# Performance work log

Measured on AMD Instinct MI355X. Metric: run time of the kernel, lower is better.

The kernel has to match this reference:

```python
import jax, jax.numpy as jnp
import numpy as np
import math

# ---------------- static setup: real Clebsch-Gordan coefficients up to L=4 ----------------
L_MAX = 4
DIM = (L_MAX + 1) ** 2  # 25 irrep components
NUM_RADIAL = 64
R_CUT = 5.0
_DEG_OF = np.repeat(np.arange(L_MAX + 1), 2 * np.arange(L_MAX + 1) + 1)  # degree of each lm slot


def _cg_complex(l1, m1, l2, m2, l3, m3):
    if m1 + m2 != m3 or l3 < abs(l1 - l2) or l3 > l1 + l2:
        return 0.0
    f = math.factorial
    pref = math.sqrt((2 * l3 + 1) * f(l1 + l2 - l3) * f(l1 - l2 + l3) * f(-l1 + l2 + l3) / f(l1 + l2 + l3 + 1))
    pref *= math.sqrt(f(l1 + m1) * f(l1 - m1) * f(l2 + m2) * f(l2 - m2) * f(l3 + m3) * f(l3 - m3))
    s = 0.0
    for k in range(l1 + l2 - l3 + 1):
        d = (k, l1 + l2 - l3 - k, l1 - m1 - k, l2 + m2 - k, l3 - l2 + m1 + k, l3 - l1 - m2 + k)
        if min(d) < 0:
            continue
        den = 1
        for x in d:
            den *= f(x)
        s += (-1.0) ** k / den
    return pref * s


def _u_mat(l):
    # complex -> real spherical harmonics change of basis
    U = np.zeros((2 * l + 1, 2 * l + 1), dtype=np.complex128)
    U[l, l] = 1.0
    rs2 = 1.0 / math.sqrt(2.0)
    for m in range(1, l + 1):
        U[l + m, l + m] = (-1.0) ** m * rs2
        U[l + m, l - m] = rs2
        U[l - m, l - m] = 1j * rs2
        U[l - m, l + m] = -1j * (-1.0) ** m * rs2
    return U


def _real_cg():
    C = np.zeros((DIM, DIM, DIM))
    U = [_u_mat(l) for l in range(L_MAX + 1)]
    for l1 in range(L_MAX + 1):
        for l2 in range(L_MAX + 1):
            for l3 in range(L_MAX + 1):
                cgc = np.zeros((2 * l1 + 1, 2 * l2 + 1, 2 * l3 + 1))
                for m1 in range(-l1, l1 + 1):
                    for m2 in range(-l2, l2 + 1):
                        m3 = m1 + m2
                        if abs(m3) <= l3:
                            cgc[l1 + m1, l2 + m2, l3 + m3] = _cg_complex(l1, m1, l2, m2, l3, m3)
                blk = np.einsum('am,bn,cp,mnp->abc', U[l1], U[l2], U[l3].conj(), cgc.astype(np.complex128))
                blk = blk.real if (l1 + l2 + l3) % 2 == 0 else blk.imag
                C[l1 * l1:l1 * l1 + 2 * l1 + 1, l2 * l2:l2 * l2 + 2 * l2 + 1, l3 * l3:l3 * l3 + 2 * l3 + 1] = blk
    return C

_CG = jnp.asarray(_real_cg(), dtype=jnp.float32)  # [25,25,25]


def real_sh(u):
    # u: [P,3] unit vectors -> [P,25] orthonormal real spherical harmonics, L<=4
    x, y, z = u[:, 0], u[:, 1], u[:, 2]
    x2, y2, z2 = x * x, y * y, z * z
    Y = [jnp.full_like(x, 0.28209479177387814),
         0.4886025119029199 * y, 0.4886025119029199 * z, 0.4886025119029199 * x,
         1.0925484305920792 * x * y, 1.0925484305920792 * y * z,
         0.31539156525252005 * (3.0 * z2 - 1.0),
         1.0925484305920792 * x * z, 0.5462742152960396 * (x2 - y2),
         0.5900435899266435 * y * (3.0 * x2 - y2), 2.890611442640554 * x * y * z,
         0.4570457994644658 * y * (5.0 * z2 - 1.0), 0.3731763325901154 * z * (5.0 * z2 - 3.0),
         0.4570457994644658 * x * (5.0 * z2 - 1.0), 1.445305721320277 * z * (x2 - y2),
         0.5900435899266435 * x * (x2 - 3.0 * y2),
         2.5033429417967046 * x * y * (x2 - y2), 1.7701307697799304 * y * z * (3.0 * x2 - y2),
         0.9461746957575601 * x * y * (7.0 * z2 - 1.0), 0.6690465435572892 * y * z * (7.0 * z2 - 3.0),
         0.10578554691520431 * (35.0 * z2 * z2 - 30.0 * z2 + 3.0),
         0.6690465435572892 * x * z * (7.0 * z2 - 3.0), 0.47308734787878004 * (x2 - y2) * (7.0 * z2 - 1.0),
         1.7701307697799304 * x * z * (x2 - 3.0 * y2),
         0.6258357354491761 * (x2 * x2 - 6.0 * x2 * y2 + y2 * y2)]
    return jnp.stack(Y, axis=-1)


def deg_dense(feat, W, b):
    Wlm = W[_DEG_OF]  # [25,Fin,Fout]
    out = jnp.einsum('plf,lfg->plg', feat, Wlm)
    return out.at[:, 0, :].add(b)


def tensor_product(a, b):
    # channelwise CG coupling: out[p,k,f] = sum_ij CG[i,j,k] a[p,i,f] b[p,j,f]
    out = jnp.zeros_like(a)
    for i in range(DIM):  # fixed structural loop over 25 lm slots, avoids [P,25,25,F] temp
        out = out + a[:, i, None, :] * jnp.einsum('jk,pjf->pkf', _CG[i], b)
    return out


def radial_basis(disp, s_j):
    # species-aware radial basis x spherical harmonics -> [P,25,F]
    r = jnp.sqrt(jnp.sum(disp * disp, axis=-1) + 1e-12)
    Y = real_sh(disp / r[:, None])
    centers = jnp.linspace(0.0, R_CUT, NUM_RADIAL, dtype=disp.dtype)
    delta = R_CUT / (NUM_RADIAL - 1)
    g = jnp.exp(-0.5 / (delta * delta) * (r[:, None] - centers) ** 2)
    env = 0.5 * (jnp.cos(jnp.pi * jnp.clip(r / R_CUT, 0.0, 1.0)) + 1.0)  # smooth cutoff
    radial = g * env[:, None] * s_j  # species-modulated radial channels [P,F]
    return Y[:, :, None] * radial[:, None, :]


def setup_inputs() -> dict:
    key = jax.random.key(0)
    ks = jax.random.split(key, 8)
    num_atoms, num_pairs, F = 2048, 32768, 64
    return {
        'atomic_numbers': jax.random.randint(ks[0], (num_atoms,), 0, 119),
        'neighbour_displacements': jax.random.normal(ks[1], (num_pairs, 3), dtype=jnp.float32),
        'neighbour_indices': jax.random.randint(ks[2], (2, num_pairs), 0, num_atoms),
        'species_embed': jax.random.normal(ks[3], (119, F), dtype=jnp.float32),
        'Wt': jax.random.normal(ks[4], (F, F), dtype=jnp.float32) / 8.0,
        'bt': jnp.zeros((F,), dtype=jnp.float32),
        'W1': jax.random.normal(ks[5], (5, F, F), dtype=jnp.float32) / 8.0,
        'b1': jnp.zeros((F,), dtype=jnp.float32),
        'W2': jax.random.normal(ks[6], (5, F, F), dtype=jnp.float32) / 8.0,
        'b2': jnp.zeros((F,), dtype=jnp.float32),
    }


def reference(atomic_numbers, neighbour_displacements, neighbour_indices, species_embed, Wt, bt, W1, b1, W2, b2):
    idx_i, idx_j = neighbour_indices[0], neighbour_indices[1]
    s_j = species_embed[atomic_numbers[idx_j]]                 # gather Z_j embedding
    y = radial_basis(neighbour_displacements, s_j)             # [P,25,F]
    # TensorDense, applied max_moment-1 = 1 time
    y = tensor_product(deg_dense(y, W1, b1), deg_dense(y, W2, b2))
    # 'emb x basis': l1=0 CG is the identity -> channelwise scaling by scalar embedding of Z_i
    emb_i = species_embed[atomic_numbers[idx_i]] @ Wt + bt
    y = y * emb_i[:, None, :]
    out = jax.ops.segment_sum(y, idx_i, num_segments=atomic_numbers.shape[0])  # scatter-sum to atoms
    # residual: scalar embedding added to the l=0 component
    emb = species_embed[atomic_numbers] @ Wt + bt
    return out.at[:, 0, :].add(emb)
```

## Files before the change

kernel.cpp:

```cpp
#include <hip/hip_runtime.h>

#define DEVINL __device__ __forceinline__

typedef __attribute__((ext_vector_type(8))) short bf16x8;
typedef __attribute__((ext_vector_type(4))) float f32x4;

constexpr int LMAX = 4;

struct Triples { int n; int l1[80], l2[80], l3[80]; };
constexpr Triples make_triples() {
  Triples T{}; T.n = 0;
  for (int a = 0; a <= LMAX; ++a)
    for (int b = 0; b <= LMAX; ++b)
      for (int c = 0; c <= LMAX; ++c) {
        int lo = a > b ? a - b : b - a;
        if (c < lo || c > a + b) continue;
        T.l1[T.n] = a; T.l2[T.n] = b; T.l3[T.n] = c; ++T.n;
      }
  return T;
}
constexpr Triples TRI = make_triples();
static_assert(TRI.n == 65, "triples");

struct ETriT { int n; signed char l1[48], l2[48], l3[48]; };
constexpr ETriT make_etri() {
  ETriT E{}; E.n = 0;
  for (int t = 0; t < TRI.n; ++t)
    if (((TRI.l1[t] + TRI.l2[t] + TRI.l3[t]) & 1) == 0) {
      E.l1[E.n] = (signed char)TRI.l1[t];
      E.l2[E.n] = (signed char)TRI.l2[t];
      E.l3[E.n] = (signed char)TRI.l3[t];
      ++E.n;
    }
  return E;
}
constexpr ETriT ETRI = make_etri();
static_assert(ETRI.n == 42, "even triples");

constexpr double FT[14] = {1., 1., 2., 6., 24., 120., 720., 5040., 40320.,
                           362880., 3628800., 39916800., 479001600., 6227020800.};

constexpr double csqrt(double x) {
  if (x <= 0.0) return 0.0;
  double y = 1.0;
  while (y * y < x) y *= 2.0;
  for (int i = 0; i < 30; ++i) y = 0.5 * (y + x / y);
  return y;
}

constexpr double cg_complex(int l1, int m1, int l2, int m2, int l3, int m3) {
  if (m1 + m2 != m3) return 0.0;
  double pref = csqrt((2.0 * l3 + 1.0) * FT[l1 + l2 - l3] * FT[l1 - l2 + l3] *
                      FT[-l1 + l2 + l3] / FT[l1 + l2 + l3 + 1]);
  pref *= csqrt(FT[l1 + m1] * FT[l1 - m1] * FT[l2 + m2] * FT[l2 - m2] *
                FT[l3 + m3] * FT[l3 - m3]);
  double s = 0.0;
  for (int k = 0; k <= l1 + l2 - l3; ++k) {
    int d3 = l1 - m1 - k, d4 = l2 + m2 - k, d5 = l3 - l2 + m1 + k, d6 = l3 - l1 - m2 + k;
    if (d3 < 0 || d4 < 0 || d5 < 0 || d6 < 0) continue;
    double den = FT[k] * FT[l1 + l2 - l3 - k] * FT[d3] * FT[d4] * FT[d5] * FT[d6];
    s += ((k & 1) ? -1.0 : 1.0) / den;
  }
  return pref * s;
}

struct CURow { int n; int m[2]; double re[2], im[2]; };
constexpr CURow cu_row(int l, int a) {
  CURow u{}; int ma = a - l;
  const double RS2 = 0.70710678118654752440;
  if (ma == 0) { u.n = 1; u.m[0] = 0; u.re[0] = 1.0; u.im[0] = 0.0; }
  else if (ma > 0) {
    u.n = 2;
    u.m[0] = ma;  u.re[0] = ((ma & 1) ? -RS2 : RS2); u.im[0] = 0.0;
    u.m[1] = -ma; u.re[1] = RS2;                     u.im[1] = 0.0;
  } else {
    int mm = -ma; u.n = 2;
    u.m[0] = -mm; u.re[0] = 0.0; u.im[0] = RS2;
    u.m[1] =  mm; u.re[1] = 0.0; u.im[1] = ((mm & 1) ? RS2 : -RS2);
  }
  return u;
}

constexpr double real_cg_entry(int l1, int a, int l2, int b, int l3, int c) {
  CURow u1 = cu_row(l1, a), u2 = cu_row(l2, b), u3 = cu_row(l3, c);
  double sre = 0.0, sim = 0.0;
  for (int x = 0; x < u1.n; ++x)
    for (int y = 0; y < u2.n; ++y)
      for (int z = 0; z < u3.n; ++z) {
        int m1 = u1.m[x], m2 = u2.m[y], m3 = u3.m[z];
        if (m1 + m2 != m3) continue;
        double cg = cg_complex(l1, m1, l2, m2, l3, m3);
        if (cg == 0.0) continue;
        double are = u1.re[x], aim = u1.im[x], bre = u2.re[y], bim = u2.im[y];
        double pre = are * bre - aim * bim, pim = are * bim + aim * bre;
        double cre = u3.re[z], cim = -u3.im[z];
        sre += (pre * cre - pim * cim) * cg;
        sim += (pre * cim + pim * cre) * cg;
      }
  return ((l1 + l2 + l3) & 1) ? sim : sre;
}

struct Y25D { double y[25]; };
constexpr Y25D csh25(double x, double y, double z) {
  Y25D Y{};
  double x2 = x * x, y2 = y * y, z2 = z * z;
  Y.y[0] = 0.28209479177387814;
  Y.y[1] = 0.4886025119029199 * y;
  Y.y[2] = 0.4886025119029199 * z;
  Y.y[3] = 0.4886025119029199 * x;
  Y.y[4] = 1.0925484305920792 * x * y;
  Y.y[5] = 1.0925484305920792 * y * z;
  Y.y[6] = 0.31539156525252005 * (3.0 * z2 - 1.0);
  Y.y[7] = 1.0925484305920792 * x * z;
  Y.y[8] = 0.5462742152960396 * (x2 - y2);
  Y.y[9] = 0.5900435899266435 * y * (3.0 * x2 - y2);
  Y.y[10] = 2.890611442640554 * x * y * z;
  Y.y[11] = 0.4570457994644658 * y * (5.0 * z2 - 1.0);
  Y.y[12] = 0.3731763325901154 * z * (5.0 * z2 - 3.0);
  Y.y[13] = 0.4570457994644658 * x * (5.0 * z2 - 1.0);
  Y.y[14] = 1.445305721320277 * z * (x2 - y2);
  Y.y[15] = 0.5900435899266435 * x * (x2 - 3.0 * y2);
  Y.y[16] = 2.5033429417967046 * x * y * (x2 - y2);
  Y.y[17] = 1.7701307697799304 * y * z * (3.0 * x2 - y2);
  Y.y[18] = 0.9461746957575601 * x * y * (7.0 * z2 - 1.0);
  Y.y[19] = 0.6690465435572892 * y * z * (7.0 * z2 - 3.0);
  Y.y[20] = 0.10578554691520431 * (35.0 * z2 * z2 - 30.0 * z2 + 3.0);
  Y.y[21] = 0.6690465435572892 * x * z * (7.0 * z2 - 3.0);
  Y.y[22] = 0.47308734787878004 * (x2 - y2) * (7.0 * z2 - 1.0);
  Y.y[23] = 1.7701307697799304 * x * z * (x2 - 3.0 * y2);
  Y.y[24] = 0.6258357354491761 * (x2 * x2 - 6.0 * x2 * y2 + y2 * y2);
  return Y;
}

constexpr double compute_A_even(int e) {
  int l1 = ETRI.l1[e], l2 = ETRI.l2[e], l3 = ETRI.l3[e];
  double ux = 0.437, uy = -0.602, uz = 0.668;
  double n = csqrt(ux * ux + uy * uy + uz * uz);
  Y25D Y = csh25(ux / n, uy / n, uz / n);
  int c0 = 2 * l3;
  double den = Y.y[l3 * l3 + c0];
  double num = 0.0;
  for (int a = 0; a < 2 * l1 + 1; ++a)
    for (int b = 0; b < 2 * l2 + 1; ++b) {
      double v = real_cg_entry(l1, a, l2, b, l3, c0);
      if (v != 0.0) num += v * Y.y[l1 * l1 + a] * Y.y[l2 * l2 + b];
    }
  return num / den;
}

template <int E> inline constexpr float A_of = (float)compute_A_even(E);
constexpr float AT42[42] = {
    A_of<0>,  A_of<1>,  A_of<2>,  A_of<3>,  A_of<4>,  A_of<5>,  A_of<6>,
    A_of<7>,  A_of<8>,  A_of<9>,  A_of<10>, A_of<11>, A_of<12>, A_of<13>,
    A_of<14>, A_of<15>, A_of<16>, A_of<17>, A_of<18>, A_of<19>, A_of<20>,
    A_of<21>, A_of<22>, A_of<23>, A_of<24>, A_of<25>, A_of<26>, A_of<27>,
    A_of<28>, A_of<29>, A_of<30>, A_of<31>, A_of<32>, A_of<33>, A_of<34>,
    A_of<35>, A_of<36>, A_of<37>, A_of<38>, A_of<39>, A_of<40>, A_of<41>};

DEVINL unsigned short f2bf(float x) {
  unsigned u = __float_as_uint(x);
  u += 0x7FFFu + ((u >> 16) & 1u);
  return (unsigned short)(u >> 16);
}

DEVINL void sh25(float x, float y, float z, float* Y) {
  float x2 = x * x, y2 = y * y, z2 = z * z;
  Y[0] = 0.28209479177387814f;
  Y[1] = 0.4886025119029199f * y;
  Y[2] = 0.4886025119029199f * z;
  Y[3] = 0.4886025119029199f * x;
  Y[4] = 1.0925484305920792f * x * y;
  Y[5] = 1.0925484305920792f * y * z;
  Y[6] = 0.31539156525252005f * (3.0f * z2 - 1.0f);
  Y[7] = 1.0925484305920792f * x * z;
  Y[8] = 0.5462742152960396f * (x2 - y2);
  Y[9] = 0.5900435899266435f * y * (3.0f * x2 - y2);
  Y[10] = 2.890611442640554f * x * y * z;
  Y[11] = 0.4570457994644658f * y * (5.0f * z2 - 1.0f);
  Y[12] = 0.3731763325901154f * z * (5.0f * z2 - 3.0f);
  Y[13] = 0.4570457994644658f * x * (5.0f * z2 - 1.0f);
  Y[14] = 1.445305721320277f * z * (x2 - y2);
  Y[15] = 0.5900435899266435f * x * (x2 - 3.0f * y2);
  Y[16] = 2.5033429417967046f * x * y * (x2 - y2);
  Y[17] = 1.7701307697799304f * y * z * (3.0f * x2 - y2);
  Y[18] = 0.9461746957575601f * x * y * (7.0f * z2 - 1.0f);
  Y[19] = 0.6690465435572892f * y * z * (7.0f * z2 - 3.0f);
  Y[20] = 0.10578554691520431f * (35.0f * z2 * z2 - 30.0f * z2 + 3.0f);
  Y[21] = 0.6690465435572892f * x * z * (7.0f * z2 - 3.0f);
  Y[22] = 0.47308734787878004f * (x2 - y2) * (7.0f * z2 - 1.0f);
  Y[23] = 1.7701307697799304f * x * z * (x2 - 3.0f * y2);
  Y[24] = 0.6258357354491761f * (x2 * x2 - 6.0f * x2 * y2 + y2 * y2);
}

__global__ void khist(const int* __restrict__ nbr, int* __restrict__ counts, int P) {
  int p = blockIdx.x * 256 + threadIdx.x;
  if (p < P) atomicAdd(&counts[nbr[p]], 1);
}

__global__ void kscan(const int* __restrict__ counts, int* __restrict__ offsets,
                      int* __restrict__ cursor, int A, int P) {
  __shared__ int sh[256];
  int t = threadIdx.x;
  int items = A / 256;
  int local[16];
  int sum = 0;
  for (int u = 0; u < items; ++u) { local[u] = sum; sum += counts[t * items + u]; }
  sh[t] = sum;
  __syncthreads();
  for (int off = 1; off < 256; off <<= 1) {
    int v = (t >= off) ? sh[t - off] : 0;
    __syncthreads();
    sh[t] += v;
    __syncthreads();
  }
  int base = sh[t] - sum;
  for (int u = 0; u < items; ++u) {
    int o = base + local[u];
    offsets[t * items + u] = o;
    cursor[t * items + u] = o;
  }
  if (t == 255) offsets[A] = P;
}

__global__ void kscat(const int* __restrict__ nbr, int* __restrict__ cursor,
                      int* __restrict__ plist, int P) {
  int p = blockIdx.x * 256 + threadIdx.x;
  if (p < P) {
    int a = nbr[p];
    int pos = atomicAdd(&cursor[a], 1);
    plist[pos] = p;
  }
}

__global__ void ktw(const float* __restrict__ W1, const float* __restrict__ W2,
                    unsigned short* __restrict__ WT) {
  int idx = blockIdx.x * 256 + threadIdx.x;
  if (idx >= 40960) return;
  int c = idx & 63, g = (idx >> 6) & 63, l = idx >> 12;
  const float* W = (l < 5) ? (W1 + (size_t)l * 4096) : (W2 + (size_t)(l - 5) * 4096);
  WT[idx] = f2bf(W[c * 64 + g]);
}

__global__ __launch_bounds__(256) void k2G(const int* __restrict__ Z,
                                           const int* __restrict__ nbr,
                                           const float* __restrict__ disp,
                                           const float* __restrict__ se,
                                           const unsigned short* __restrict__ WT,
                                           const float* __restrict__ b1,
                                           const float* __restrict__ b2,
                                           float* __restrict__ Gout, int P) {
  __shared__ alignas(16) unsigned short rad[128 * 72];
  const int p0 = blockIdx.x * 128;
  const int g0 = blockIdx.y * 16;
  const int t = threadIdx.x;

  {
    int pl = t >> 1, half = t & 1;
    int p = p0 + pl;
    int zj = Z[nbr[P + p]];
    float dx = disp[3 * p], dy = disp[3 * p + 1], dz = disp[3 * p + 2];
    float r = sqrtf(dx * dx + dy * dy + dz * dz + 1e-12f);
    float env = 0.5f * (__cosf(3.14159265358979f * fminf(r * 0.2f, 1.0f)) + 1.0f);
    const float delta = 5.0f / 63.0f;
    const float w = 0.5f / (delta * delta);
    int c0 = half * 32;
    const float4* s4 = (const float4*)(se + (size_t)zj * 64 + c0);
    unsigned* radw = (unsigned*)rad;
#pragma unroll
    for (int i = 0; i < 8; ++i) {
      float4 s = s4[i];
      float d0 = r - (float)(c0 + 4 * i + 0) * delta;
      float d1 = r - (float)(c0 + 4 * i + 1) * delta;
      float d2 = r - (float)(c0 + 4 * i + 2) * delta;
      float d3 = r - (float)(c0 + 4 * i + 3) * delta;
      float v0 = __expf(-w * d0 * d0) * env * s.x;
      float v1 = __expf(-w * d1 * d1) * env * s.y;
      float v2 = __expf(-w * d2 * d2) * env * s.z;
      float v3 = __expf(-w * d3 * d3) * env * s.w;
      radw[pl * 36 + half * 16 + 2 * i] =
          (unsigned)f2bf(v0) | ((unsigned)f2bf(v1) << 16);
      radw[pl * 36 + half * 16 + 2 * i + 1] =
          (unsigned)f2bf(v2) | ((unsigned)f2bf(v3) << 16);
    }
  }
  __syncthreads();

  const int lane = t & 63, wv = t >> 6;
  const int n = lane & 15, quad = lane >> 4;
  const int g = g0 + n;
  const float invY0 = 3.5449077018110318f;

  bf16x8 B[10][2];
#pragma unroll
  for (int l = 0; l < 10; ++l)
#pragma unroll
    for (int kk = 0; kk < 2; ++kk)
      B[l][kk] = *(const bf16x8*)(WT + (((size_t)l * 64 + g) * 64 + kk * 32 + quad * 8));

  float bb1 = b1[g] * invY0, bb2 = b2[g] * invY0;

  const int m0 = wv * 32;
#pragma unroll
  for (int mt = 0; mt < 2; ++mt) {
    int row = m0 + mt * 16 + n;
    bf16x8 A0 = *(const bf16x8*)(rad + row * 72 + quad * 8);
    bf16x8 A1 = *(const bf16x8*)(rad + row * 72 + 32 + quad * 8);
    f32x4 C[10];
#pragma unroll
    for (int l = 0; l < 10; ++l) C[l] = (f32x4){0.f, 0.f, 0.f, 0.f};
#pragma unroll
    for (int l = 0; l < 10; ++l) {
      C[l] = __builtin_amdgcn_mfma_f32_16x16x32_bf16(A0, B[l][0], C[l], 0, 0, 0);
      C[l] = __builtin_amdgcn_mfma_f32_16x16x32_bf16(A1, B[l][1], C[l], 0, 0, 0);
    }
#pragma unroll
    for (int r = 0; r < 4; ++r) { C[0][r] += bb1; C[5][r] += bb2; }

    f32x4 Gac[5];
#pragma unroll
    for (int l = 0; l < 5; ++l) Gac[l] = (f32x4){0.f, 0.f, 0.f, 0.f};
#pragma unroll
    for (int l1 = 0; l1 < 5; ++l1)
#pragma unroll
      for (int l2 = 0; l2 < 5; ++l2) {
        f32x4 pr = C[l1] * C[5 + l2];
#pragma unroll
        for (int e = 0; e < 42; ++e)
          if ((int)ETRI.l1[e] == l1 && (int)ETRI.l2[e] == l2)
            Gac[(int)ETRI.l3[e]] += AT42[e] * pr;
      }

    int prow = p0 + m0 + mt * 16 + quad * 4;
#pragma unroll
    for (int l3 = 0; l3 < 5; ++l3)
#pragma unroll
      for (int r = 0; r < 4; ++r)
        Gout[(size_t)(prow + r) * 320 + l3 * 64 + g] = Gac[l3][r];
  }
}

__global__ __launch_bounds__(256) void k3(const float* __restrict__ G,
                                          const float* __restrict__ disp,
                                          const int* __restrict__ Z,
                                          const float* __restrict__ se,
                                          const float* __restrict__ Wt,
                                          const float* __restrict__ bt,
                                          const int* __restrict__ offsets,
                                          const int* __restrict__ plist,
                                          float* __restrict__ out, int P) {
  __shared__ float red[3 * 1600];
  int atom = blockIdx.x;
  int f = threadIdx.x & 63, wv = threadIdx.x >> 6;
  float acc[25];
#pragma unroll
  for (int k = 0; k < 25; ++k) acc[k] = 0.f;
  int beg = offsets[atom], end = offsets[atom + 1];

  for (int q = beg + wv; q < end; q += 4) {
    int p = __builtin_amdgcn_readfirstlane(plist[q]);
    float dx = disp[3 * p], dy = disp[3 * p + 1], dz = disp[3 * p + 2];
    const float* Gp = G + (size_t)p * 320 + f;
    float g0 = Gp[0], g1 = Gp[64], g2 = Gp[128], g3 = Gp[192], g4 = Gp[256];
    float r = sqrtf(dx * dx + dy * dy + dz * dz + 1e-12f);
    float inv = 1.0f / r;
    float Y[25];
    sh25(dx * inv, dy * inv, dz * inv, Y);
    acc[0] = fmaf(Y[0], g0, acc[0]);
#pragma unroll
    for (int k = 1; k < 4; ++k)   acc[k] = fmaf(Y[k], g1, acc[k]);
#pragma unroll
    for (int k = 4; k < 9; ++k)   acc[k] = fmaf(Y[k], g2, acc[k]);
#pragma unroll
    for (int k = 9; k < 16; ++k)  acc[k] = fmaf(Y[k], g3, acc[k]);
#pragma unroll
    for (int k = 16; k < 25; ++k) acc[k] = fmaf(Y[k], g4, acc[k]);
  }

  if (wv > 0) {
#pragma unroll
    for (int k = 0; k < 25; ++k) red[(wv - 1) * 1600 + k * 64 + f] = acc[k];
  }
  __syncthreads();
  if (wv == 0) {
#pragma unroll
    for (int k = 0; k < 25; ++k)
      acc[k] += red[k * 64 + f] + red[1600 + k * 64 + f] + red[3200 + k * 64 + f];
    int z = Z[atom];
    float e = bt[f];
    for (int c = 0; c < 64; ++c)
      e = fmaf(se[(size_t)z * 64 + c], Wt[(size_t)c * 64 + f], e);
#pragma unroll
    for (int k = 0; k < 25; ++k)
      out[(size_t)atom * 1600 + (size_t)k * 64 + f] = fmaf(acc[k], e, (k == 0) ? e : 0.f);
  }
}

static inline size_t align256(size_t x) { return (x + 255) & ~(size_t)255; }

extern "C" void kernel_launch(void* const* d_in, const int* in_sizes, int n_in,
                              void* d_out, int out_size, void* d_ws, size_t ws_size,
                              hipStream_t stream) {
  const int*   Z    = (const int*)d_in[0];
  const float* disp = (const float*)d_in[1];
  const int*   nbr  = (const int*)d_in[2];
  const float* se   = (const float*)d_in[3];
  const float* Wt   = (const float*)d_in[4];
  const float* bt   = (const float*)d_in[5];
  const float* W1   = (const float*)d_in[6];
  const float* b1   = (const float*)d_in[7];
  const float* W2   = (const float*)d_in[8];
  const float* b2   = (const float*)d_in[9];
  float* out = (float*)d_out;

  const int A = in_sizes[0];
  const int P = in_sizes[1] / 3;

  char* ws = (char*)d_ws;
  size_t o = 0;
  float*          G    = (float*)(ws + o);          o += align256((size_t)P * 320 * 4);
  unsigned short* WT   = (unsigned short*)(ws + o); o += align256((size_t)40960 * 2);
  int* counts  = (int*)(ws + o); o += align256((size_t)A * 4);
  int* offsets = (int*)(ws + o); o += align256((size_t)(A + 1) * 4);
  int* cursor  = (int*)(ws + o); o += align256((size_t)A * 4);
  int* plist   = (int*)(ws + o); o += align256((size_t)P * 4);
  (void)ws_size; (void)n_in; (void)out_size;

  int pb = (P + 255) / 256;

  hipMemsetAsync(counts, 0, (size_t)A * 4, stream);
  khist<<<pb, 256, 0, stream>>>(nbr, counts, P);
  kscan<<<1, 256, 0, stream>>>(counts, offsets, cursor, A, P);
  kscat<<<pb, 256, 0, stream>>>(nbr, cursor, plist, P);
  ktw<<<160, 256, 0, stream>>>(W1, W2, WT);
  dim3 g2((unsigned)(P / 128), 4, 1);
  k2G<<<g2, 256, 0, stream>>>(Z, nbr, disp, se, WT, b1, b2, G, P);
  k3<<<A, 256, 0, stream>>>(G, disp, Z, se, Wt, bt, offsets, plist, out, P);
}
```

Before: 135.6 us.

## Fold CSR build into G kernel block and store G as bf16

Removes the memset, histogram, scan and scatter kernels and has block 0 of the G-computation kernel build the per-atom neighbour offsets and pair list in shared memory while the other blocks compute G. The intermediate G buffer is also stored as bf16 instead of fp32, halving its write and gather traffic in the final reduction kernel. This saves several launches and global atomics, but it serialises the whole CSR build onto a single block and adds bf16 rounding error to G. The shared-memory count array assumes A fits within the existing shared buffer.

```diff
diff --git a/kernel.cpp b/kernel.cpp
--- a/kernel.cpp
+++ b/kernel.cpp
@@ -162,6 +162,7 @@
   u += 0x7FFFu + ((u >> 16) & 1u);
   return (unsigned short)(u >> 16);
 }
+DEVINL float bf2f(unsigned short b) { return __uint_as_float((unsigned)b << 16); }
 
 DEVINL void sh25(float x, float y, float z, float* Y) {
   float x2 = x * x, y2 = y * y, z2 = z * z;
@@ -192,46 +193,6 @@
   Y[24] = 0.6258357354491761f * (x2 * x2 - 6.0f * x2 * y2 + y2 * y2);
 }
 
-__global__ void khist(const int* __restrict__ nbr, int* __restrict__ counts, int P) {
-  int p = blockIdx.x * 256 + threadIdx.x;
-  if (p < P) atomicAdd(&counts[nbr[p]], 1);
-}
-
-__global__ void kscan(const int* __restrict__ counts, int* __restrict__ offsets,
-                      int* __restrict__ cursor, int A, int P) {
-  __shared__ int sh[256];
-  int t = threadIdx.x;
-  int items = A / 256;
-  int local[16];
-  int sum = 0;
-  for (int u = 0; u < items; ++u) { local[u] = sum; sum += counts[t * items + u]; }
-  sh[t] = sum;
-  __syncthreads();
-  for (int off = 1; off < 256; off <<= 1) {
-    int v = (t >= off) ? sh[t - off] : 0;
-    __syncthreads();
-    sh[t] += v;
-    __syncthreads();
-  }
-  int base = sh[t] - sum;
-  for (int u = 0; u < items; ++u) {
-    int o = base + local[u];
-    offsets[t * items + u] = o;
-    cursor[t * items + u] = o;
-  }
-  if (t == 255) offsets[A] = P;
-}
-
-__global__ void kscat(const int* __restrict__ nbr, int* __restrict__ cursor,
-                      int* __restrict__ plist, int P) {
-  int p = blockIdx.x * 256 + threadIdx.x;
-  if (p < P) {
-    int a = nbr[p];
-    int pos = atomicAdd(&cursor[a], 1);
-    plist[pos] = p;
-  }
-}
-
 __global__ void ktw(const float* __restrict__ W1, const float* __restrict__ W2,
                     unsigned short* __restrict__ WT) {
   int idx = blockIdx.x * 256 + threadIdx.x;
@@ -241,18 +202,61 @@
   WT[idx] = f2bf(W[c * 64 + g]);
 }
 
-__global__ __launch_bounds__(256) void k2G(const int* __restrict__ Z,
+__global__ __launch_bounds__(256) void kc2(const int* __restrict__ Z,
                                            const int* __restrict__ nbr,
                                            const float* __restrict__ disp,
                                            const float* __restrict__ se,
                                            const unsigned short* __restrict__ WT,
                                            const float* __restrict__ b1,
                                            const float* __restrict__ b2,
-                                           float* __restrict__ Gout, int P) {
-  __shared__ alignas(16) unsigned short rad[128 * 72];
-  const int p0 = blockIdx.x * 128;
-  const int g0 = blockIdx.y * 16;
+                                           unsigned short* __restrict__ Gout,
+                                           int* __restrict__ offsets,
+                                           int* __restrict__ plist,
+                                           int A, int P) {
+  __shared__ alignas(16) unsigned short smem[128 * 72];
   const int t = threadIdx.x;
+
+  if (blockIdx.x == 0) {
+    int* cnt = (int*)smem;
+    __shared__ int sh[256];
+    for (int i = t; i < A; i += 256) cnt[i] = 0;
+    __syncthreads();
+    for (int q = t; q < P; q += 256) atomicAdd(&cnt[nbr[q]], 1);
+    __syncthreads();
+    const int items = A / 256;
+    int local[16];
+    int sum = 0;
+    for (int u = 0; u < items; ++u) { local[u] = sum; sum += cnt[t * items + u]; }
+    sh[t] = sum;
+    __syncthreads();
+    for (int off = 1; off < 256; off <<= 1) {
+      int v = (t >= off) ? sh[t - off] : 0;
+      __syncthreads();
+      sh[t] += v;
+      __syncthreads();
+    }
+    int base = sh[t] - sum;
+    int offv[16];
+    for (int u = 0; u < items; ++u) {
+      offv[u] = base + local[u];
+      offsets[t * items + u] = offv[u];
+    }
+    if (t == 255) offsets[A] = P;
+    __syncthreads();
+    for (int u = 0; u < items; ++u) cnt[t * items + u] = offv[u];
+    __syncthreads();
+    for (int q = t; q < P; q += 256) {
+      int a = nbr[q];
+      int pos = atomicAdd(&cnt[a], 1);
+      plist[pos] = q;
+    }
+    return;
+  }
+
+  unsigned short* rad = smem;
+  const int bid = blockIdx.x - 1;
+  const int p0 = (bid >> 2) * 128;
+  const int g0 = (bid & 3) * 16;
 
   {
     int pl = t >> 1, half = t & 1;
@@ -335,11 +339,11 @@
     for (int l3 = 0; l3 < 5; ++l3)
 #pragma unroll
       for (int r = 0; r < 4; ++r)
-        Gout[(size_t)(prow + r) * 320 + l3 * 64 + g] = Gac[l3][r];
-  }
-}
-
-__global__ __launch_bounds__(256) void k3(const float* __restrict__ G,
+        Gout[(size_t)(prow + r) * 320 + l3 * 64 + g] = f2bf(Gac[l3][r]);
+  }
+}
+
+__global__ __launch_bounds__(256) void k3(const unsigned short* __restrict__ G,
                                           const float* __restrict__ disp,
                                           const int* __restrict__ Z,
                                           const float* __restrict__ se,
@@ -359,8 +363,9 @@
   for (int q = beg + wv; q < end; q += 4) {
     int p = __builtin_amdgcn_readfirstlane(plist[q]);
     float dx = disp[3 * p], dy = disp[3 * p + 1], dz = disp[3 * p + 2];
-    const float* Gp = G + (size_t)p * 320 + f;
-    float g0 = Gp[0], g1 = Gp[64], g2 = Gp[128], g3 = Gp[192], g4 = Gp[256];
+    const unsigned short* Gp = G + (size_t)p * 320 + f;
+    float g0 = bf2f(Gp[0]),   g1 = bf2f(Gp[64]), g2 = bf2f(Gp[128]);
+    float g3 = bf2f(Gp[192]), g4 = bf2f(Gp[256]);
     float r = sqrtf(dx * dx + dy * dy + dz * dz + 1e-12f);
     float inv = 1.0f / r;
     float Y[25];
@@ -417,22 +422,14 @@
 
   char* ws = (char*)d_ws;
   size_t o = 0;
-  float*          G    = (float*)(ws + o);          o += align256((size_t)P * 320 * 4);
-  unsigned short* WT   = (unsigned short*)(ws + o); o += align256((size_t)40960 * 2);
-  int* counts  = (int*)(ws + o); o += align256((size_t)A * 4);
+  unsigned short* G  = (unsigned short*)(ws + o); o += align256((size_t)P * 320 * 2);
+  unsigned short* WT = (unsigned short*)(ws + o); o += align256((size_t)40960 * 2);
   int* offsets = (int*)(ws + o); o += align256((size_t)(A + 1) * 4);
-  int* cursor  = (int*)(ws + o); o += align256((size_t)A * 4);
   int* plist   = (int*)(ws + o); o += align256((size_t)P * 4);
   (void)ws_size; (void)n_in; (void)out_size;
 
-  int pb = (P + 255) / 256;
-
-  hipMemsetAsync(counts, 0, (size_t)A * 4, stream);
-  khist<<<pb, 256, 0, stream>>>(nbr, counts, P);
-  kscan<<<1, 256, 0, stream>>>(counts, offsets, cursor, A, P);
-  kscat<<<pb, 256, 0, stream>>>(nbr, cursor, plist, P);
   ktw<<<160, 256, 0, stream>>>(W1, W2, WT);
-  dim3 g2((unsigned)(P / 128), 4, 1);
-  k2G<<<g2, 256, 0, stream>>>(Z, nbr, disp, se, WT, b1, b2, G, P);
+  kc2<<<1 + (P / 128) * 4, 256, 0, stream>>>(Z, nbr, disp, se, WT, b1, b2,
+                                             G, offsets, plist, A, P);
   k3<<<A, 256, 0, stream>>>(G, disp, Z, se, Wt, bt, offsets, plist, out, P);
 }
```

Result: slower. 181.0 us (+33.5%).
